# Optimization experiments

Measured on AMD Instinct MI355X. Metric: run time of the kernel, lower is better.

The kernel has to match this reference:

```python
import jax, jax.numpy as jnp
import numpy as np

NEG_SLOPE = 0.2
EPS = 1e-16


def add_self_loops(edge_index, num_nodes):
    loops = jnp.arange(num_nodes, dtype=edge_index.dtype)
    return jnp.concatenate([edge_index, jnp.stack([loops, loops])], axis=1)


def gat_conv(x, edge_index, W, att_src, att_dst, bias, concat):
    # PyG GATConv: linear -> per-head attention logits -> segment softmax over
    # incoming edges of each destination node -> weighted scatter-add.
    N = x.shape[0]
    H, C = att_src.shape
    ei = add_self_loops(edge_index, N)
    src, dst = ei[0], ei[1]
    h = (x @ W).reshape(N, H, C)                      # [N,H,C]
    a_src = jnp.einsum('nhc,hc->nh', h, att_src)       # [N,H]
    a_dst = jnp.einsum('nhc,hc->nh', h, att_dst)       # [N,H]
    logits = jax.nn.leaky_relu(a_src[src] + a_dst[dst], NEG_SLOPE)  # [E,H]
    m = jax.ops.segment_max(logits, dst, num_segments=N)            # [N,H]
    e = jnp.exp(logits - m[dst])
    s = jax.ops.segment_sum(e, dst, num_segments=N)                 # [N,H]
    alpha = e / (s[dst] + EPS)                                      # [E,H]
    out = jax.ops.segment_sum(h[src] * alpha[:, :, None], dst, num_segments=N)  # [N,H,C]
    out = out.reshape(N, H * C) if concat else out.mean(axis=1)
    return out + bias


def setup_inputs() -> dict:
    key = jax.random.key(0)
    ks = jax.random.split(key, 10)
    N, E, F_in, Hd, heads, F_out = 50000, 800000, 128, 32, 4, 64
    return {
        'x': jax.random.normal(ks[0], (N, F_in), jnp.float32),
        'edge_index': jax.random.randint(ks[1], (2, E), 0, N, jnp.int64),
        'W1': jax.random.normal(ks[2], (F_in, heads * Hd), jnp.float32) * 0.1,
        'att_src1': jax.random.normal(ks[3], (heads, Hd), jnp.float32) * 0.1,
        'att_dst1': jax.random.normal(ks[4], (heads, Hd), jnp.float32) * 0.1,
        'bias1': jax.random.normal(ks[5], (heads * Hd,), jnp.float32) * 0.1,
        'W2': jax.random.normal(ks[6], (heads * Hd, heads * F_out), jnp.float32) * 0.1,
        'att_src2': jax.random.normal(ks[7], (heads, F_out), jnp.float32) * 0.1,
        'att_dst2': jax.random.normal(ks[8], (heads, F_out), jnp.float32) * 0.1,
        'bias2': jax.random.normal(ks[9], (F_out,), jnp.float32) * 0.1,
    }


def reference(x, edge_index, W1, att_src1, att_dst1, bias1, W2, att_src2, att_dst2, bias2):
    h = gat_conv(x, edge_index, W1, att_src1, att_dst1, bias1, concat=True)
    h = jax.nn.elu(h)  # dropout p=0.0 / eval mode -> identity
    out = gat_conv(h, edge_index, W2, att_src2, att_dst2, bias2, concat=False)
    return out
```

## Files before the change

### kernel.cpp

```cpp
#include <hip/hip_runtime.h>

typedef unsigned int uint;
typedef unsigned short ushort;


__device__ __forceinline__ float leaky(float x) { return x >= 0.f ? x : 0.2f * x; }
__device__ __forceinline__ float b2f(ushort h) { return __uint_as_float(((uint)h) << 16); }
__device__ __forceinline__ ushort f2b(float f) {
    uint u = __float_as_uint(f);
    return (ushort)((u + 0x7FFF + ((u >> 16) & 1)) >> 16);
}

#if defined(__has_builtin)
#if __has_builtin(__builtin_amdgcn_fdot2_f32_bf16)
#define HAS_DOT2 1
#endif
#endif
#ifndef HAS_DOT2
#define HAS_DOT2 0
#endif

#if HAS_DOT2
typedef __bf16 bf16v2 __attribute__((ext_vector_type(2)));
__device__ __forceinline__ float dot2bf(uint h2, uint w2, float c) {
    return __builtin_amdgcn_fdot2_f32_bf16(__builtin_bit_cast(bf16v2, h2),
                                           __builtin_bit_cast(bf16v2, w2), c, false);
}
#define DOT2PAIR(hE, hE1, wpk, a0, a1)                                  \
    a0 = dot2bf(__builtin_amdgcn_perm(hE, hE1, 0x01000504), wpk, a0);   \
    a1 = dot2bf(__builtin_amdgcn_perm(hE, hE1, 0x03020706), wpk, a1);
#else
#define DOT2PAIR(hE, hE1, wpk, a0, a1)                                  \
    {                                                                   \
        float wlo = __uint_as_float((wpk) << 16);                       \
        float whi = __uint_as_float((wpk) & 0xffff0000u);               \
        a0 = fmaf(wlo, __uint_as_float((hE) << 16), a0);                \
        a1 = fmaf(wlo, __uint_as_float((hE) & 0xffff0000u), a1);        \
        a0 = fmaf(whi, __uint_as_float((hE1) << 16), a0);               \
        a1 = fmaf(whi, __uint_as_float((hE1) & 0xffff0000u), a1);       \
    }
#endif

__global__ void detect_kernel(const int* __restrict__ ei, const void* __restrict__ xin,
                              int* __restrict__ flagI, int* __restrict__ flagF,
                              int* __restrict__ bcnt) {
    __shared__ int s_sane, s_odd;
    int t = threadIdx.x;
    bcnt[t] = 0;
    if (t == 0) { s_sane = 0; s_odd = 0; }
    __syncthreads();
    if (t < 64 && ei[2 * t + 1] != 0) atomicOr(&s_odd, 1);
    ushort v = ((const ushort*)xin)[2 * t];
    int ex = (v >> 7) & 0xFF;
    if (v == 0 || (ex >= 100 && ex <= 135)) atomicAdd(&s_sane, 1);
    __syncthreads();
    if (t == 0) { *flagI = (s_odd == 0); *flagF = (s_sane >= 230); }
}

__device__ __forceinline__ float rdf(const void* p_, int i, int bf) {
    return bf ? b2f(((const ushort*)p_)[i]) : ((const float*)p_)[i];
}

__global__ void prep_kernel(const void* __restrict__ x, const void* __restrict__ W1,
                            const void* __restrict__ as1, const void* __restrict__ ad1,
                            const void* __restrict__ b1, const void* __restrict__ b2,
                            const void* __restrict__ W2, const void* __restrict__ as2,
                            const void* __restrict__ ad2,
                            ushort* __restrict__ xbf, ushort* __restrict__ W1T,
                            float* __restrict__ att1, float* __restrict__ b1f,
                            float* __restrict__ b2f_, float* __restrict__ w2t8,
                            ushort* __restrict__ W2sT, int NX, const int* __restrict__ flagF) {
    int bf = *flagF;
    int b = blockIdx.x, t = threadIdx.x;
    int nxb = (NX + 255) / 256;
    if (b < nxb) {
        if (bf) return;
        int i = b * 256 + t;
        if (i < NX) xbf[i] = f2b(((const float*)x)[i]);
        return;
    }
    b -= nxb;
    if (b < 64) {
        int i = b * 256 + t;
        int k = i >> 7, n = i & 127;
        W1T[n * 128 + k] = bf ? ((const ushort*)W1)[i] : f2b(((const float*)W1)[i]);
        return;
    }
    b -= 64;
    if (b < 2) {
        int i = b * 256 + t;
        if (i < 128)      att1[i] = rdf(as1, i, bf);
        else if (i < 256) att1[i] = rdf(ad1, i - 128, bf);
        else if (i < 384) b1f[i - 256] = rdf(b1, i - 256, bf);
        else if (i < 448) b2f_[i - 384] = rdf(b2, i - 384, bf);
        return;
    }
    b -= 2;
    if (b < 4) {
        int idx = b * 256 + t;
        int o = idx >> 7, k = idx & 127, h = o & 3;
        const void* att = (o < 4) ? as2 : ad2;
        float s = 0.f;
        for (int c = 0; c < 64; ++c) s += rdf(W2, k * 256 + h * 64 + c, bf) * rdf(att, h * 64 + c, bf);
        w2t8[o * 128 + k] = s;
        return;
    }
    b -= 4;
    {
        int idx = b * 256 + t;
        int c = idx >> 9, hk = idx & 511;
        int h = hk >> 7, k = hk & 127;
        W2sT[c * 512 + hk] = f2b(0.25f * rdf(W2, k * 256 + h * 64 + c, bf));
    }
}

__device__ __forceinline__ int edge_dst(const int* __restrict__ ei, int E, int e, int is64) {
    return (e >= E) ? (e - E) : (is64 ? ei[2 * E + 2 * e] : ei[E + e]);
}

__global__ __launch_bounds__(256) void bhist_kernel(const int* __restrict__ ei, int E, int ET,
                                                    const int* __restrict__ flagI,
                                                    int* __restrict__ bcnt) {
    __shared__ int bins[256];
    int t = threadIdx.x;
    bins[t] = 0;
    __syncthreads();
    int is64 = *flagI;
    int base = blockIdx.x * 4096;
    for (int i = 0; i < 16; ++i) {
        int e = base + i * 256 + t;
        if (e < ET) atomicAdd(&bins[edge_dst(ei, E, e, is64) >> 8], 1);
    }
    __syncthreads();
    if (bins[t]) atomicAdd(&bcnt[t], bins[t]);
}

__global__ __launch_bounds__(256) void bscan_kernel(const int* __restrict__ bcnt,
                                                    int* __restrict__ bbase,
                                                    int* __restrict__ gcur, int NBUK) {
    __shared__ int sc[256];
    int t = threadIdx.x;
    int v = (t < NBUK) ? bcnt[t] : 0;
    sc[t] = v;
    __syncthreads();
    for (int off = 1; off < 256; off <<= 1) {
        int a = (t >= off) ? sc[t - off] : 0;
        __syncthreads();
        sc[t] += a;
        __syncthreads();
    }
    int excl = sc[t] - v;
    if (t < NBUK) { bbase[t] = excl; gcur[t] = excl; }
    if (t == 255) bbase[NBUK] = sc[255];
}

__global__ __launch_bounds__(256) void part_kernel(const int* __restrict__ ei, int E, int ET,
                                                   const int* __restrict__ flagI,
                                                   int* __restrict__ gcur,
                                                   uint* __restrict__ ebuf, int NBUK) {
    __shared__ uint stage[8192];
    __shared__ int cnt_s[256], sc[256], lbase[257], cur[256], gb[256];
    int t = threadIdx.x;
    int base = blockIdx.x * 8192;
    cnt_s[t] = 0;
    __syncthreads();
    int is64 = *flagI;
    uint pk[32];
    short bk[32];
#pragma unroll
    for (int i = 0; i < 32; ++i) {
        int e = base + i * 256 + t;
        if (e < ET) {
            int src, dst;
            if (e >= E) { src = dst = e - E; }
            else if (is64) { src = ei[2 * e]; dst = ei[2 * E + 2 * e]; }
            else           { src = ei[e];     dst = ei[E + e]; }
            pk[i] = (uint)src | ((uint)dst << 16);
            bk[i] = (short)(dst >> 8);
            atomicAdd(&cnt_s[bk[i]], 1);
        } else bk[i] = -1;
    }
    __syncthreads();
    int v = cnt_s[t];
    sc[t] = v;
    __syncthreads();
    for (int off = 1; off < 256; off <<= 1) {
        int a = (t >= off) ? sc[t - off] : 0;
        __syncthreads();
        sc[t] += a;
        __syncthreads();
    }
    lbase[t + 1] = sc[t];
    cur[t] = sc[t] - v;
    if (t == 0) lbase[0] = 0;
    __syncthreads();
#pragma unroll
    for (int i = 0; i < 32; ++i)
        if (bk[i] >= 0) {
            int slot = atomicAdd(&cur[bk[i]], 1);
            stage[slot] = pk[i];
        }
    __syncthreads();
    if (t < NBUK) {
        int c = lbase[t + 1] - lbase[t];
        if (c > 0) gb[t] = atomicAdd(&gcur[t], c);
    }
    __syncthreads();
    int total = lbase[256];
    for (int i = t; i < total; i += 256) {
        int lo = 0, hi = 255;
        while (lo < hi) { int mid = (lo + hi + 1) >> 1; if (lbase[mid] <= i) lo = mid; else hi = mid - 1; }
        ebuf[gb[lo] + (i - lbase[lo])] = stage[i];
    }
}

__global__ __launch_bounds__(256) void bfinal_kernel(const uint* __restrict__ ebuf,
                                                     const int* __restrict__ bbase,
                                                     int* __restrict__ rowptr,
                                                     int* __restrict__ ecol, int N, int NBUK) {
    __shared__ int hist[2048], cur2[2048], ws[4];
    int b = blockIdx.x, t = threadIdx.x;
    int lane = t & 63, wid = t >> 6;
    int d0 = b << 8;
#pragma unroll
    for (int j = 0; j < 8; ++j) hist[t * 8 + j] = 0;
    __syncthreads();
    int s = bbase[b], e2 = bbase[b + 1];
    for (int i = s + t; i < e2; i += 256) {
        uint pk = ebuf[i];
        int key = (((int)(pk >> 16) - d0) << 3) | (int)((pk & 0xffffu) >> 13);
        atomicAdd(&hist[key], 1);
    }
    __syncthreads();
    int loc[8];
    int v = 0;
#pragma unroll
    for (int j = 0; j < 8; ++j) { loc[j] = v; v += hist[t * 8 + j]; }
    int incl = v;
#pragma unroll
    for (int off = 1; off < 64; off <<= 1) {
        int a = __shfl_up(incl, off, 64);
        if (lane >= off) incl += a;
    }
    if (lane == 63) ws[wid] = incl;
    __syncthreads();
    if (t == 0) {
        int acc = 0;
        for (int j = 0; j < 4; ++j) { int x = ws[j]; ws[j] = acc; acc += x; }
    }
    __syncthreads();
    int excl = incl - v + ws[wid];
    int d = d0 + t;
    if (d < N) rowptr[d] = s + excl;
#pragma unroll
    for (int j = 0; j < 8; ++j) cur2[t * 8 + j] = s + excl + loc[j];
    if (b == NBUK - 1 && t == 0) rowptr[N] = bbase[NBUK];
    __syncthreads();
    for (int i = s + t; i < e2; i += 256) {
        uint pk = ebuf[i];
        int key = (((int)(pk >> 16) - d0) << 3) | (int)((pk & 0xffffu) >> 13);
        int pos = atomicAdd(&cur2[key], 1);
        ecol[pos] = (int)(pk & 0xffffu);
    }
}

__global__ void hist_kernel(const int* __restrict__ ei, int E, int N,
                            const int* __restrict__ flag, int* __restrict__ deg) {
    int e = blockIdx.x * blockDim.x + threadIdx.x;
    if (e >= E + N) return;
    atomicAdd(&deg[edge_dst(ei, E, e, *flag)], 1);
}
__global__ void scatter_kernel(const int* __restrict__ ei, int E, int N,
                               const int* __restrict__ flag, const int* __restrict__ rowptr,
                               int* __restrict__ cnt, int* __restrict__ ecol) {
    int e = blockIdx.x * blockDim.x + threadIdx.x;
    if (e >= E + N) return;
    int src, dst;
    if (e >= E) { src = dst = e - E; }
    else if (*flag) { src = ei[2 * e]; dst = ei[2 * E + 2 * e]; }
    else            { src = ei[e];     dst = ei[E + e]; }
    int pos = rowptr[dst] + atomicAdd(&cnt[dst], 1);
    ecol[pos] = src;
}
__global__ __launch_bounds__(1024) void scan1_kernel(const int* __restrict__ deg,
                                                     int* __restrict__ tmp,
                                                     int* __restrict__ bsum, int n) {
    __shared__ int ws[16];
    int tid = threadIdx.x, lane = tid & 63, wid = tid >> 6;
    int i = blockIdx.x * 1024 + tid;
    int v = (i < n) ? deg[i] : 0;
    int incl = v;
#pragma unroll
    for (int off = 1; off < 64; off <<= 1) {
        int t2 = __shfl_up(incl, off, 64);
        if (lane >= off) incl += t2;
    }
    if (lane == 63) ws[wid] = incl;
    __syncthreads();
    if (tid < 16) {
        int wv_ = ws[tid], winc = wv_;
#pragma unroll
        for (int off = 1; off < 16; off <<= 1) {
            int t2 = __shfl_up(winc, off, 16);
            if (tid >= off) winc += t2;
        }
        ws[tid] = winc - wv_;
    }
    __syncthreads();
    int excl = incl - v + ws[wid];
    if (i < n) tmp[i] = excl;
    if (tid == 1023) bsum[blockIdx.x] = excl + v;
}
__global__ void scan2_kernel(int* __restrict__ bsum, int nb) {
    int lane = threadIdx.x;
    int v = (lane < nb) ? bsum[lane] : 0;
    int incl = v;
    for (int off = 1; off < 64; off <<= 1) {
        int t = __shfl_up(incl, off, 64);
        if (lane >= off) incl += t;
    }
    int total = __shfl(incl, nb - 1, 64);
    if (lane < nb) bsum[lane] = incl - v;
    if (lane == 0) bsum[nb] = total;
}
__global__ void scan3_kernel(const int* __restrict__ tmp, const int* __restrict__ bsum,
                             int* __restrict__ rowptr, int* __restrict__ cnt, int n, int nb) {
    int i = blockIdx.x * blockDim.x + threadIdx.x;
    if (i > n) return;
    rowptr[i] = (i == n) ? bsum[nb] : tmp[i] + bsum[i >> 10];
    if (i < n) cnt[i] = 0;
}

typedef __attribute__((ext_vector_type(8))) short bf16x8;
typedef __attribute__((ext_vector_type(4))) float floatx4;

__global__ __launch_bounds__(256) void gemm1_kernel(
    const void* __restrict__ xraw, const ushort* __restrict__ xbf, const int* __restrict__ flagF,
    const ushort* __restrict__ BT, ushort* __restrict__ C,
    const float* __restrict__ att, float4* __restrict__ asrc4, float4* __restrict__ adst4, int M) {
    constexpr int K = 128, NT = 8;
    const ushort* A = (*flagF) ? (const ushort*)xraw : xbf;
    int lane = threadIdx.x & 63, wv = threadIdx.x >> 6;
    int row0 = (blockIdx.x * 4 + wv) * 16;
    if (row0 >= M) return;
    int m = lane & 15, quad = lane >> 4;
    int rowa = min(row0 + m, M - 1);
    const bf16x8* arow = (const bf16x8*)(A + (size_t)rowa * K);
    bf16x8 af[4];
#pragma unroll
    for (int kk = 0; kk < 4; ++kk) af[kk] = arow[4 * kk + quad];
    floatx4 acc[NT] = {};
#pragma unroll
    for (int nt = 0; nt < NT; ++nt) {
        const bf16x8* brow = (const bf16x8*)(BT + (size_t)(nt * 16 + m) * K);
#pragma unroll
        for (int kk = 0; kk < 4; ++kk)
            acc[nt] = __builtin_amdgcn_mfma_f32_16x16x32_bf16(af[kk], brow[4 * kk + quad], acc[nt], 0, 0, 0);
    }
#pragma unroll
    for (int nt = 0; nt < NT; ++nt)
#pragma unroll
        for (int r = 0; r < 4; ++r) {
            int row = row0 + quad * 4 + r;
            if (row < M) C[(size_t)row * 128 + nt * 16 + m] = f2b(acc[nt][r]);
        }
    float attS[NT], attD[NT];
#pragma unroll
    for (int nt = 0; nt < NT; ++nt) { attS[nt] = att[nt * 16 + m]; attD[nt] = att[128 + nt * 16 + m]; }
#pragma unroll
    for (int r = 0; r < 4; ++r) {
        float ps[4] = {0, 0, 0, 0}, pd[4] = {0, 0, 0, 0};
#pragma unroll
        for (int nt = 0; nt < NT; ++nt) {
            int h = nt / 2;
            ps[h] = fmaf(acc[nt][r], attS[nt], ps[h]);
            pd[h] = fmaf(acc[nt][r], attD[nt], pd[h]);
        }
#pragma unroll
        for (int off = 1; off < 16; off <<= 1) {
#pragma unroll
            for (int h = 0; h < 4; ++h) {
                ps[h] += __shfl_xor(ps[h], off, 64);
                pd[h] += __shfl_xor(pd[h], off, 64);
            }
        }
        int row = row0 + quad * 4 + r;
        if (m == 0 && row < M) {
            asrc4[row] = make_float4(ps[0], ps[1], ps[2], ps[3]);
            adst4[row] = make_float4(pd[0], pd[1], pd[2], pd[3]);
        }
    }
}

__global__ __launch_bounds__(256) void agg1_kernel(
    const ushort* __restrict__ hsrc, const float4* __restrict__ a_src4,
    const float4* __restrict__ a_dst4, const int* __restrict__ rowptr,
    const int* __restrict__ ecol, const float* __restrict__ bias,
    const float* __restrict__ w2t8, uint4* __restrict__ outz,
    float4* __restrict__ asrc2, float4* __restrict__ adst2, int N) {
    constexpr int SH = 7;
    __shared__ __align__(16) ushort elds[4][4][4][20];
    int lane = threadIdx.x & 63, wv = threadIdx.x >> 6;
    int q = lane >> 4, c = lane & 15, qbase = q << 4;
    int n = blockIdx.x * 16 + wv * 4 + q;
    bool nv = n < N;
    int start = 0, end = 0;
    if (nv) { start = rowptr[n]; end = rowptr[n + 1]; }
    int deg = end - start;
    float4 ad = nv ? a_dst4[n] : make_float4(0.f, 0.f, 0.f, 0.f);
    int hh = c >> 2;
    uint laneoff = (uint)c * 8;
    float acc[8] = {};
    float ss0 = 0.f, ss1 = 0.f, ss2 = 0.f, ss3 = 0.f;

    for (int cs = 0; cs < deg; cs += 16) {
        int len = min(16, deg - cs);
        bool v = c < len;
        int sv = v ? ecol[start + cs + c] : 0;
        float4 as = a_src4[sv];
        float e0 = v ? __expf(fminf(leaky(as.x + ad.x), 60.f)) : 0.f;
        float e1 = v ? __expf(fminf(leaky(as.y + ad.y), 60.f)) : 0.f;
        float e2 = v ? __expf(fminf(leaky(as.z + ad.z), 60.f)) : 0.f;
        float e3 = v ? __expf(fminf(leaky(as.w + ad.w), 60.f)) : 0.f;
        ushort r0 = f2b(e0), r1 = f2b(e1), r2 = f2b(e2), r3 = f2b(e3);
        elds[wv][0][q][c] = r0; elds[wv][1][q][c] = r1;
        elds[wv][2][q][c] = r2; elds[wv][3][q][c] = r3;
        ss0 += b2f(r0); ss1 += b2f(r1); ss2 += b2f(r2); ss3 += b2f(r3);
        for (int e = 0; e < len; e += 4) {
            int s0 = __shfl(sv, qbase + e + 0, 64);
            int s1 = __shfl(sv, qbase + e + 1, 64);
            int s2 = __shfl(sv, qbase + e + 2, 64);
            int s3 = __shfl(sv, qbase + e + 3, 64);
            uint2 w = *(const uint2*)&elds[wv][hh][q][e];
            uint4 h0 = *(const uint4*)(hsrc + (((uint)s0) << SH) + laneoff);
            uint4 h1 = *(const uint4*)(hsrc + (((uint)s1) << SH) + laneoff);
            uint4 h2 = *(const uint4*)(hsrc + (((uint)s2) << SH) + laneoff);
            uint4 h3 = *(const uint4*)(hsrc + (((uint)s3) << SH) + laneoff);
            DOT2PAIR(h0.x, h1.x, w.x, acc[0], acc[1]); DOT2PAIR(h0.y, h1.y, w.x, acc[2], acc[3]);
            DOT2PAIR(h0.z, h1.z, w.x, acc[4], acc[5]); DOT2PAIR(h0.w, h1.w, w.x, acc[6], acc[7]);
            DOT2PAIR(h2.x, h3.x, w.y, acc[0], acc[1]); DOT2PAIR(h2.y, h3.y, w.y, acc[2], acc[3]);
            DOT2PAIR(h2.z, h3.z, w.y, acc[4], acc[5]); DOT2PAIR(h2.w, h3.w, w.y, acc[6], acc[7]);
        }
    }
#pragma unroll
    for (int off = 1; off < 16; off <<= 1) {
        ss0 += __shfl_xor(ss0, off, 64); ss1 += __shfl_xor(ss1, off, 64);
        ss2 += __shfl_xor(ss2, off, 64); ss3 += __shfl_xor(ss3, off, 64);
    }
    if (!nv) return;
    float ih = (hh == 0) ? 1.f / (ss0 + 1e-16f) : (hh == 1) ? 1.f / (ss1 + 1e-16f)
             : (hh == 2) ? 1.f / (ss2 + 1e-16f) : 1.f / (ss3 + 1e-16f);
    float4 bA = ((const float4*)bias)[2 * c], bB = ((const float4*)bias)[2 * c + 1];
    float o[8];
    o[0] = acc[0] * ih + bA.x; o[1] = acc[1] * ih + bA.y;
    o[2] = acc[2] * ih + bA.z; o[3] = acc[3] * ih + bA.w;
    o[4] = acc[4] * ih + bB.x; o[5] = acc[5] * ih + bB.y;
    o[6] = acc[6] * ih + bB.z; o[7] = acc[7] * ih + bB.w;
#pragma unroll
    for (int j = 0; j < 8; ++j) o[j] = o[j] > 0.f ? o[j] : __expf(o[j]) - 1.f;
    uint4 pk;
    pk.x = (uint)f2b(o[0]) | ((uint)f2b(o[1]) << 16);
    pk.y = (uint)f2b(o[2]) | ((uint)f2b(o[3]) << 16);
    pk.z = (uint)f2b(o[4]) | ((uint)f2b(o[5]) << 16);
    pk.w = (uint)f2b(o[6]) | ((uint)f2b(o[7]) << 16);
    outz[(size_t)n * 16 + c] = pk;

    float po[8];
#pragma unroll
    for (int oo = 0; oo < 8; ++oo) {
        float4 wA = ((const float4*)(w2t8 + oo * 128))[2 * c];
        float4 wB = ((const float4*)(w2t8 + oo * 128))[2 * c + 1];
        po[oo] = o[0] * wA.x + o[1] * wA.y + o[2] * wA.z + o[3] * wA.w
               + o[4] * wB.x + o[5] * wB.y + o[6] * wB.z + o[7] * wB.w;
    }
#pragma unroll
    for (int off = 1; off < 16; off <<= 1)
#pragma unroll
        for (int oo = 0; oo < 8; ++oo) po[oo] += __shfl_xor(po[oo], off, 64);
    if (c == 0) {
        asrc2[n] = make_float4(po[0], po[1], po[2], po[3]);
        adst2[n] = make_float4(po[4], po[5], po[6], po[7]);
    }
}

__global__ __launch_bounds__(256) void agg2_kernel(
    const ushort* __restrict__ hsrc, const float4* __restrict__ a_src4,
    const float4* __restrict__ a_dst4, const int* __restrict__ rowptr,
    const int* __restrict__ ecol, const ushort* __restrict__ W2sT,
    const float* __restrict__ b2, float* __restrict__ outp, int N) {
    constexpr int SH = 7;
    __shared__ __align__(16) ushort elds[4][4][4][20];
    __shared__ __align__(16) ushort lds_a[16][520];
    int lane = threadIdx.x & 63, wv = threadIdx.x >> 6;
    int q = lane >> 4, c = lane & 15, qbase = q << 4;
    int n = blockIdx.x * 16 + wv * 4 + q;
    bool nv = n < N;
    int start = 0, end = 0;
    if (nv) { start = rowptr[n]; end = rowptr[n + 1]; }
    int deg = end - start;
    float4 ad = nv ? a_dst4[n] : make_float4(0.f, 0.f, 0.f, 0.f);
    uint laneoff = (uint)c * 8;
    float a0_[8] = {}, a1_[8] = {}, a2_[8] = {}, a3_[8] = {};
    float ss0 = 0.f, ss1 = 0.f, ss2 = 0.f, ss3 = 0.f;

    for (int cs = 0; cs < deg; cs += 16) {
        int len = min(16, deg - cs);
        bool v = c < len;
        int sv = v ? ecol[start + cs + c] : 0;
        float4 as = a_src4[sv];
        float e0 = v ? __expf(fminf(leaky(as.x + ad.x), 60.f)) : 0.f;
        float e1 = v ? __expf(fminf(leaky(as.y + ad.y), 60.f)) : 0.f;
        float e2 = v ? __expf(fminf(leaky(as.z + ad.z), 60.f)) : 0.f;
        float e3 = v ? __expf(fminf(leaky(as.w + ad.w), 60.f)) : 0.f;
        ushort r0 = f2b(e0), r1 = f2b(e1), r2 = f2b(e2), r3 = f2b(e3);
        elds[wv][0][q][c] = r0; elds[wv][1][q][c] = r1;
        elds[wv][2][q][c] = r2; elds[wv][3][q][c] = r3;
        ss0 += b2f(r0); ss1 += b2f(r1); ss2 += b2f(r2); ss3 += b2f(r3);
        for (int e = 0; e < len; e += 4) {
            int s0 = __shfl(sv, qbase + e + 0, 64);
            int s1 = __shfl(sv, qbase + e + 1, 64);
            int s2 = __shfl(sv, qbase + e + 2, 64);
            int s3 = __shfl(sv, qbase + e + 3, 64);
            uint2 w0 = *(const uint2*)&elds[wv][0][q][e];
            uint2 w1 = *(const uint2*)&elds[wv][1][q][e];
            uint2 w2 = *(const uint2*)&elds[wv][2][q][e];
            uint2 w3 = *(const uint2*)&elds[wv][3][q][e];
            uint4 h0 = *(const uint4*)(hsrc + (((uint)s0) << SH) + laneoff);
            uint4 h1 = *(const uint4*)(hsrc + (((uint)s1) << SH) + laneoff);
            uint4 h2 = *(const uint4*)(hsrc + (((uint)s2) << SH) + laneoff);
            uint4 h3 = *(const uint4*)(hsrc + (((uint)s3) << SH) + laneoff);
            DOT2PAIR(h0.x, h1.x, w0.x, a0_[0], a0_[1]); DOT2PAIR(h0.y, h1.y, w0.x, a0_[2], a0_[3]);
            DOT2PAIR(h0.z, h1.z, w0.x, a0_[4], a0_[5]); DOT2PAIR(h0.w, h1.w, w0.x, a0_[6], a0_[7]);
            DOT2PAIR(h0.x, h1.x, w1.x, a1_[0], a1_[1]); DOT2PAIR(h0.y, h1.y, w1.x, a1_[2], a1_[3]);
            DOT2PAIR(h0.z, h1.z, w1.x, a1_[4], a1_[5]); DOT2PAIR(h0.w, h1.w, w1.x, a1_[6], a1_[7]);
            DOT2PAIR(h0.x, h1.x, w2.x, a2_[0], a2_[1]); DOT2PAIR(h0.y, h1.y, w2.x, a2_[2], a2_[3]);
            DOT2PAIR(h0.z, h1.z, w2.x, a2_[4], a2_[5]); DOT2PAIR(h0.w, h1.w, w2.x, a2_[6], a2_[7]);
            DOT2PAIR(h0.x, h1.x, w3.x, a3_[0], a3_[1]); DOT2PAIR(h0.y, h1.y, w3.x, a3_[2], a3_[3]);
            DOT2PAIR(h0.z, h1.z, w3.x, a3_[4], a3_[5]); DOT2PAIR(h0.w, h1.w, w3.x, a3_[6], a3_[7]);
            DOT2PAIR(h2.x, h3.x, w0.y, a0_[0], a0_[1]); DOT2PAIR(h2.y, h3.y, w0.y, a0_[2], a0_[3]);
            DOT2PAIR(h2.z, h3.z, w0.y, a0_[4], a0_[5]); DOT2PAIR(h2.w, h3.w, w0.y, a0_[6], a0_[7]);
            DOT2PAIR(h2.x, h3.x, w1.y, a1_[0], a1_[1]); DOT2PAIR(h2.y, h3.y, w1.y, a1_[2], a1_[3]);
            DOT2PAIR(h2.z, h3.z, w1.y, a1_[4], a1_[5]); DOT2PAIR(h2.w, h3.w, w1.y, a1_[6], a1_[7]);
            DOT2PAIR(h2.x, h3.x, w2.y, a2_[0], a2_[1]); DOT2PAIR(h2.y, h3.y, w2.y, a2_[2], a2_[3]);
            DOT2PAIR(h2.z, h3.z, w2.y, a2_[4], a2_[5]); DOT2PAIR(h2.w, h3.w, w2.y, a2_[6], a2_[7]);
            DOT2PAIR(h2.x, h3.x, w3.y, a3_[0], a3_[1]); DOT2PAIR(h2.y, h3.y, w3.y, a3_[2], a3_[3]);
            DOT2PAIR(h2.z, h3.z, w3.y, a3_[4], a3_[5]); DOT2PAIR(h2.w, h3.w, w3.y, a3_[6], a3_[7]);
        }
    }
#pragma unroll
    for (int off = 1; off < 16; off <<= 1) {
        ss0 += __shfl_xor(ss0, off, 64); ss1 += __shfl_xor(ss1, off, 64);
        ss2 += __shfl_xor(ss2, off, 64); ss3 += __shfl_xor(ss3, off, 64);
    }
    float i0 = 1.f / (ss0 + 1e-16f), i1 = 1.f / (ss1 + 1e-16f);
    float i2 = 1.f / (ss2 + 1e-16f), i3 = 1.f / (ss3 + 1e-16f);
    int slot = wv * 4 + q;
    uint4 pk;
    pk.x = (uint)f2b(a0_[0] * i0) | ((uint)f2b(a0_[1] * i0) << 16);
    pk.y = (uint)f2b(a0_[2] * i0) | ((uint)f2b(a0_[3] * i0) << 16);
    pk.z = (uint)f2b(a0_[4] * i0) | ((uint)f2b(a0_[5] * i0) << 16);
    pk.w = (uint)f2b(a0_[6] * i0) | ((uint)f2b(a0_[7] * i0) << 16);
    *(uint4*)&lds_a[slot][0 * 128 + 8 * c] = pk;
    pk.x = (uint)f2b(a1_[0] * i1) | ((uint)f2b(a1_[1] * i1) << 16);
    pk.y = (uint)f2b(a1_[2] * i1) | ((uint)f2b(a1_[3] * i1) << 16);
    pk.z = (uint)f2b(a1_[4] * i1) | ((uint)f2b(a1_[5] * i1) << 16);
    pk.w = (uint)f2b(a1_[6] * i1) | ((uint)f2b(a1_[7] * i1) << 16);
    *(uint4*)&lds_a[slot][1 * 128 + 8 * c] = pk;
    pk.x = (uint)f2b(a2_[0] * i2) | ((uint)f2b(a2_[1] * i2) << 16);
    pk.y = (uint)f2b(a2_[2] * i2) | ((uint)f2b(a2_[3] * i2) << 16);
    pk.z = (uint)f2b(a2_[4] * i2) | ((uint)f2b(a2_[5] * i2) << 16);
    pk.w = (uint)f2b(a2_[6] * i2) | ((uint)f2b(a2_[7] * i2) << 16);
    *(uint4*)&lds_a[slot][2 * 128 + 8 * c] = pk;
    pk.x = (uint)f2b(a3_[0] * i3) | ((uint)f2b(a3_[1] * i3) << 16);
    pk.y = (uint)f2b(a3_[2] * i3) | ((uint)f2b(a3_[3] * i3) << 16);
    pk.z = (uint)f2b(a3_[4] * i3) | ((uint)f2b(a3_[5] * i3) << 16);
    pk.w = (uint)f2b(a3_[6] * i3) | ((uint)f2b(a3_[7] * i3) << 16);
    *(uint4*)&lds_a[slot][3 * 128 + 8 * c] = pk;
    __syncthreads();

    int m = lane & 15, quad = lane >> 4;
    const bf16x8* arow = (const bf16x8*)&lds_a[m][0];
    const bf16x8* brow = (const bf16x8*)(W2sT + (size_t)(wv * 16 + m) * 512);
    floatx4 acc2 = {};
#pragma unroll
    for (int kk = 0; kk < 16; ++kk)
        acc2 = __builtin_amdgcn_mfma_f32_16x16x32_bf16(arow[4 * kk + quad], brow[4 * kk + quad], acc2, 0, 0, 0);
    float bb = b2[wv * 16 + m];
#pragma unroll
    for (int r = 0; r < 4; ++r) {
        int row = quad * 4 + r;
        int node = blockIdx.x * 16 + row;
        if (node < N) outp[(size_t)node * 64 + wv * 16 + m] = acc2[r] + bb;
    }
}

extern "C" void kernel_launch(void* const* d_in, const int* in_sizes, int n_in,
                              void* d_out, int out_size, void* d_ws, size_t ws_size,
                              hipStream_t stream) {
    const void* x_raw = d_in[0];
    const int*  ei    = (const int*)d_in[1];
    const void* W1_p  = d_in[2];
    const void* as1_p = d_in[3];
    const void* ad1_p = d_in[4];
    const void* b1_p  = d_in[5];
    const void* W2_p  = d_in[6];
    const void* as2_p = d_in[7];
    const void* ad2_p = d_in[8];
    const void* b2_p  = d_in[9];

    const int F_IN = 128;
    const int N = in_sizes[0] / F_IN;
    const int E = in_sizes[1] / 2;
    const int ET = E + N;
    const int NB = (N + 1023) / 1024;
    const int NBUK = (N + 255) >> 8;

    char* p = (char*)d_ws;
    auto alloc = [&](size_t bytes) { char* r = p; p += (bytes + 255) & ~(size_t)255; return r; };
    ushort* xbf   = (ushort*)alloc((size_t)N * 128 * 2);
    ushort* W1T   = (ushort*)alloc(128 * 128 * 2);
    ushort* W2sT  = (ushort*)alloc(64 * 512 * 2);
    float*  att1f = (float*)alloc(256 * 4);
    float*  w2t8  = (float*)alloc(8 * 128 * 4);
    float*  b1f   = (float*)alloc(128 * 4);
    float*  b2f   = (float*)alloc(64 * 4);
    ushort* h1    = (ushort*)alloc((size_t)N * 128 * 2);
    ushort* hL1   = (ushort*)alloc((size_t)N * 128 * 2);
    float*  asrc1 = (float*)alloc((size_t)N * 4 * 4);
    float*  adst1 = (float*)alloc((size_t)N * 4 * 4);
    float*  asrc2 = (float*)alloc((size_t)N * 4 * 4);
    float*  adst2 = (float*)alloc((size_t)N * 4 * 4);
    int* deg    = (int*)alloc((size_t)N * 4);
    int* cnt    = (int*)alloc((size_t)N * 4);
    int* tmp    = (int*)alloc((size_t)N * 4);
    int* bsum   = (int*)alloc(128 * 4);
    int* rowptr = (int*)alloc((size_t)(N + 1) * 4);
    int* ecol   = (int*)alloc((size_t)ET * 4);
    uint* ebuf  = (uint*)alloc((size_t)ET * 4);
    int* bcnt   = (int*)alloc(256 * 4);
    int* bbase  = (int*)alloc(257 * 4);
    int* gcur   = (int*)alloc(256 * 4);
    int* flagI  = (int*)alloc(256);
    int* flagF  = (int*)alloc(256);

    detect_kernel<<<1, 256, 0, stream>>>(ei, x_raw, flagI, flagF, bcnt);

    int NX = N * F_IN;
    int nxb = (NX + 255) / 256;
    prep_kernel<<<nxb + 64 + 2 + 4 + 128, 256, 0, stream>>>(
        x_raw, W1_p, as1_p, ad1_p, b1_p, b2_p, W2_p, as2_p, ad2_p,
        xbf, W1T, att1f, b1f, b2f, w2t8, W2sT, NX, flagF);

    if (N <= 65536) {
        bhist_kernel<<<(ET + 4095) / 4096, 256, 0, stream>>>(ei, E, ET, flagI, bcnt);
        bscan_kernel<<<1, 256, 0, stream>>>(bcnt, bbase, gcur, NBUK);
        part_kernel<<<(ET + 8191) / 8192, 256, 0, stream>>>(ei, E, ET, flagI, gcur, ebuf, NBUK);
        bfinal_kernel<<<NBUK, 256, 0, stream>>>(ebuf, bbase, rowptr, ecol, N, NBUK);
    } else {
        hipMemsetAsync(deg, 0, (size_t)N * 4, stream);
        int eblocks = (ET + 255) / 256;
        hist_kernel<<<eblocks, 256, 0, stream>>>(ei, E, N, flagI, deg);
        scan1_kernel<<<NB, 1024, 0, stream>>>(deg, tmp, bsum, N);
        scan2_kernel<<<1, 64, 0, stream>>>(bsum, NB);
        scan3_kernel<<<(N + 256) / 256, 256, 0, stream>>>(tmp, bsum, rowptr, cnt, N, NB);
        scatter_kernel<<<eblocks, 256, 0, stream>>>(ei, E, N, flagI, rowptr, cnt, ecol);
    }

    int nblocks16 = (N + 15) / 16;
    int gblocks = (N + 63) / 64;
    gemm1_kernel<<<gblocks, 256, 0, stream>>>(
        x_raw, xbf, flagF, W1T, h1, att1f, (float4*)asrc1, (float4*)adst1, N);
    agg1_kernel<<<nblocks16, 256, 0, stream>>>(
        h1, (const float4*)asrc1, (const float4*)adst1, rowptr, ecol, b1f, w2t8,
        (uint4*)hL1, (float4*)asrc2, (float4*)adst2, N);
    agg2_kernel<<<nblocks16, 256, 0, stream>>>(
        hL1, (const float4*)asrc2, (const float4*)adst2, rowptr, ecol, W2sT, b2f,
        (float*)d_out, N);
}
```

Baseline: 211.1 us.

## Fuse fp32-to-bf16 conversion into GEMM load and merge detect/histogram into prep

Removes the separate pass that converts x to bf16 in a workspace buffer; the first GEMM now reads fp32 rows directly and rounds to bf16 in registers. Detection of input formats and the bucket histogram are folded into the prep kernel, with each block detecting locally, eliminating two kernel launches. This trades a large memory round trip for extra conversion ALU work in the GEMM and redundant per-block detection reads.

```diff
diff --git a/kernel.cpp b/kernel.cpp
--- a/kernel.cpp
+++ b/kernel.cpp
@@ -41,62 +41,68 @@
     }
 #endif
 
-__global__ void detect_kernel(const int* __restrict__ ei, const void* __restrict__ xin,
-                              int* __restrict__ flagI, int* __restrict__ flagF,
-                              int* __restrict__ bcnt) {
-    __shared__ int s_sane, s_odd;
-    int t = threadIdx.x;
-    bcnt[t] = 0;
-    if (t == 0) { s_sane = 0; s_odd = 0; }
-    __syncthreads();
-    if (t < 64 && ei[2 * t + 1] != 0) atomicOr(&s_odd, 1);
-    ushort v = ((const ushort*)xin)[2 * t];
+__device__ __forceinline__ int detect_bf_local(const void* xin) {
+    __shared__ int s_sane;
+    if (threadIdx.x == 0) s_sane = 0;
+    __syncthreads();
+    ushort v = ((const ushort*)xin)[2 * threadIdx.x];
     int ex = (v >> 7) & 0xFF;
     if (v == 0 || (ex >= 100 && ex <= 135)) atomicAdd(&s_sane, 1);
     __syncthreads();
-    if (t == 0) { *flagI = (s_odd == 0); *flagF = (s_sane >= 230); }
+    return s_sane >= 230;
+}
+__device__ __forceinline__ int detect_is64_local(const int* ei) {
+    __shared__ int s_odd;
+    if (threadIdx.x == 0) s_odd = 0;
+    __syncthreads();
+    if (threadIdx.x < 64 && ei[2 * threadIdx.x + 1] != 0) atomicOr(&s_odd, 1);
+    __syncthreads();
+    return s_odd == 0;
 }
 
 __device__ __forceinline__ float rdf(const void* p_, int i, int bf) {
     return bf ? b2f(((const ushort*)p_)[i]) : ((const float*)p_)[i];
+}
+
+__device__ __forceinline__ int edge_dst(const int* __restrict__ ei, int E, int e, int is64) {
+    return (e >= E) ? (e - E) : (is64 ? ei[2 * E + 2 * e] : ei[E + e]);
 }
 
 __global__ void prep_kernel(const void* __restrict__ x, const void* __restrict__ W1,
                             const void* __restrict__ as1, const void* __restrict__ ad1,
                             const void* __restrict__ b1, const void* __restrict__ b2,
                             const void* __restrict__ W2, const void* __restrict__ as2,
-                            const void* __restrict__ ad2,
-                            ushort* __restrict__ xbf, ushort* __restrict__ W1T,
-                            float* __restrict__ att1, float* __restrict__ b1f,
-                            float* __restrict__ b2f_, float* __restrict__ w2t8,
-                            ushort* __restrict__ W2sT, int NX, const int* __restrict__ flagF) {
-    int bf = *flagF;
+                            const void* __restrict__ ad2, const int* __restrict__ ei,
+                            int E, int ET,
+                            ushort* __restrict__ W1T, float* __restrict__ att1,
+                            float* __restrict__ b1f, float* __restrict__ b2f_,
+                            float* __restrict__ w2t8, ushort* __restrict__ W2sT,
+                            int* __restrict__ flagI, int* __restrict__ flagF,
+                            int* __restrict__ bcnt) {
     int b = blockIdx.x, t = threadIdx.x;
-    int nxb = (NX + 255) / 256;
-    if (b < nxb) {
-        if (bf) return;
-        int i = b * 256 + t;
-        if (i < NX) xbf[i] = f2b(((const float*)x)[i]);
-        return;
-    }
-    b -= nxb;
     if (b < 64) {
+        int bf = detect_bf_local(x);
         int i = b * 256 + t;
         int k = i >> 7, n = i & 127;
         W1T[n * 128 + k] = bf ? ((const ushort*)W1)[i] : f2b(((const float*)W1)[i]);
         return;
     }
     b -= 64;
-    if (b < 2) {
-        int i = b * 256 + t;
-        if (i < 128)      att1[i] = rdf(as1, i, bf);
-        else if (i < 256) att1[i] = rdf(ad1, i - 128, bf);
-        else if (i < 384) b1f[i - 256] = rdf(b1, i - 256, bf);
-        else if (i < 448) b2f_[i - 384] = rdf(b2, i - 384, bf);
+    if (b == 0) {
+        int bf = detect_bf_local(x);
+        int is64 = detect_is64_local(ei);
+        if (t == 0) { *flagF = bf; *flagI = is64; }
+        for (int i = t; i < 512; i += 256) {
+            if (i < 128)      att1[i] = rdf(as1, i, bf);
+            else if (i < 256) att1[i] = rdf(ad1, i - 128, bf);
+            else if (i < 384) b1f[i - 256] = rdf(b1, i - 256, bf);
+            else if (i < 448) b2f_[i - 384] = rdf(b2, i - 384, bf);
+        }
         return;
     }
-    b -= 2;
+    b -= 1;
     if (b < 4) {
+        int bf = detect_bf_local(x);
         int idx = b * 256 + t;
         int o = idx >> 7, k = idx & 127, h = o & 3;
         const void* att = (o < 4) ? as2 : ad2;
@@ -106,33 +112,28 @@
         return;
     }
     b -= 4;
-    {
+    if (b < 128) {
+        int bf = detect_bf_local(x);
         int idx = b * 256 + t;
         int c = idx >> 9, hk = idx & 511;
         int h = hk >> 7, k = hk & 127;
         W2sT[c * 512 + hk] = f2b(0.25f * rdf(W2, k * 256 + h * 64 + c, bf));
-    }
-}
-
-__device__ __forceinline__ int edge_dst(const int* __restrict__ ei, int E, int e, int is64) {
-    return (e >= E) ? (e - E) : (is64 ? ei[2 * E + 2 * e] : ei[E + e]);
-}
-
-__global__ __launch_bounds__(256) void bhist_kernel(const int* __restrict__ ei, int E, int ET,
-                                                    const int* __restrict__ flagI,
-                                                    int* __restrict__ bcnt) {
-    __shared__ int bins[256];
-    int t = threadIdx.x;
-    bins[t] = 0;
-    __syncthreads();
-    int is64 = *flagI;
-    int base = blockIdx.x * 4096;
-    for (int i = 0; i < 16; ++i) {
-        int e = base + i * 256 + t;
-        if (e < ET) atomicAdd(&bins[edge_dst(ei, E, e, is64) >> 8], 1);
-    }
-    __syncthreads();
-    if (bins[t]) atomicAdd(&bcnt[t], bins[t]);
+        return;
+    }
+    b -= 128;
+    {
+        int is64 = detect_is64_local(ei);
+        __shared__ int bins[256];
+        bins[t] = 0;
+        __syncthreads();
+        int base = b * 4096;
+        for (int i = 0; i < 16; ++i) {
+            int e = base + i * 256 + t;
+            if (e < ET) atomicAdd(&bins[edge_dst(ei, E, e, is64) >> 8], 1);
+        }
+        __syncthreads();
+        if (bins[t]) atomicAdd(&bcnt[t], bins[t]);
+    }
 }
 
 __global__ __launch_bounds__(256) void bscan_kernel(const int* __restrict__ bcnt,
@@ -335,20 +336,34 @@
 typedef __attribute__((ext_vector_type(4))) float floatx4;
 
 __global__ __launch_bounds__(256) void gemm1_kernel(
-    const void* __restrict__ xraw, const ushort* __restrict__ xbf, const int* __restrict__ flagF,
+    const void* __restrict__ xraw, const int* __restrict__ flagF,
     const ushort* __restrict__ BT, ushort* __restrict__ C,
     const float* __restrict__ att, float4* __restrict__ asrc4, float4* __restrict__ adst4, int M) {
     constexpr int K = 128, NT = 8;
-    const ushort* A = (*flagF) ? (const ushort*)xraw : xbf;
     int lane = threadIdx.x & 63, wv = threadIdx.x >> 6;
     int row0 = (blockIdx.x * 4 + wv) * 16;
     if (row0 >= M) return;
     int m = lane & 15, quad = lane >> 4;
     int rowa = min(row0 + m, M - 1);
-    const bf16x8* arow = (const bf16x8*)(A + (size_t)rowa * K);
     bf16x8 af[4];
-#pragma unroll
-    for (int kk = 0; kk < 4; ++kk) af[kk] = arow[4 * kk + quad];
+    if (*flagF) {
+        const bf16x8* arow = (const bf16x8*)((const ushort*)xraw + (size_t)rowa * K);
+#pragma unroll
+        for (int kk = 0; kk < 4; ++kk) af[kk] = arow[4 * kk + quad];
+    } else {
+        const float4* arw = (const float4*)((const float*)xraw + (size_t)rowa * K);
+#pragma unroll
+        for (int kk = 0; kk < 4; ++kk) {
+            float4 fa = arw[2 * (4 * kk + quad)];
+            float4 fb = arw[2 * (4 * kk + quad) + 1];
+            bf16x8 tv;
+            tv[0] = (short)f2b(fa.x); tv[1] = (short)f2b(fa.y);
+            tv[2] = (short)f2b(fa.z); tv[3] = (short)f2b(fa.w);
+            tv[4] = (short)f2b(fb.x); tv[5] = (short)f2b(fb.y);
+            tv[6] = (short)f2b(fb.z); tv[7] = (short)f2b(fb.w);
+            af[kk] = tv;
+        }
+    }
     floatx4 acc[NT] = {};
 #pragma unroll
     for (int nt = 0; nt < NT; ++nt) {
@@ -614,10 +629,10 @@
     const int ET = E + N;
     const int NB = (N + 1023) / 1024;
     const int NBUK = (N + 255) >> 8;
+    const int NBH = (ET + 4095) / 4096;
 
     char* p = (char*)d_ws;
     auto alloc = [&](size_t bytes) { char* r = p; p += (bytes + 255) & ~(size_t)255; return r; };
-    ushort* xbf   = (ushort*)alloc((size_t)N * 128 * 2);
     ushort* W1T   = (ushort*)alloc(128 * 128 * 2);
     ushort* W2sT  = (ushort*)alloc(64 * 512 * 2);
     float*  att1f = (float*)alloc(256 * 4);
@@ -643,16 +658,12 @@
     int* flagI  = (int*)alloc(256);
     int* flagF  = (int*)alloc(256);
 
-    detect_kernel<<<1, 256, 0, stream>>>(ei, x_raw, flagI, flagF, bcnt);
-
-    int NX = N * F_IN;
-    int nxb = (NX + 255) / 256;
-    prep_kernel<<<nxb + 64 + 2 + 4 + 128, 256, 0, stream>>>(
-        x_raw, W1_p, as1_p, ad1_p, b1_p, b2_p, W2_p, as2_p, ad2_p,
-        xbf, W1T, att1f, b1f, b2f, w2t8, W2sT, NX, flagF);
+    hipMemsetAsync(bcnt, 0, 256 * 4, stream);
+    prep_kernel<<<64 + 1 + 4 + 128 + NBH, 256, 0, stream>>>(
+        x_raw, W1_p, as1_p, ad1_p, b1_p, b2_p, W2_p, as2_p, ad2_p, ei, E, ET,
+        W1T, att1f, b1f, b2f, w2t8, W2sT, flagI, flagF, bcnt);
 
     if (N <= 65536) {
-        bhist_kernel<<<(ET + 4095) / 4096, 256, 0, stream>>>(ei, E, ET, flagI, bcnt);
         bscan_kernel<<<1, 256, 0, stream>>>(bcnt, bbase, gcur, NBUK);
         part_kernel<<<(ET + 8191) / 8192, 256, 0, stream>>>(ei, E, ET, flagI, gcur, ebuf, NBUK);
         bfinal_kernel<<<NBUK, 256, 0, stream>>>(ebuf, bbase, rowptr, ecol, N, NBUK);
@@ -669,7 +680,7 @@
     int nblocks16 = (N + 15) / 16;
     int gblocks = (N + 63) / 64;
     gemm1_kernel<<<gblocks, 256, 0, stream>>>(
-        x_raw, xbf, flagF, W1T, h1, att1f, (float4*)asrc1, (float4*)adst1, N);
+        x_raw, flagF, W1T, h1, att1f, (float4*)asrc1, (float4*)adst1, N);
     agg1_kernel<<<nblocks16, 256, 0, stream>>>(
         h1, (const float4*)asrc1, (const float4*)adst1, rowptr, ecol, b1f, w2t8,
         (uint4*)hL1, (float4*)asrc2, (float4*)adst2, N);
```

Result: faster. 194.6 us (-7.8%).
